# Kernel tuning notes

Measured on AMD Instinct MI355X. Metric: run time of the kernel, lower is better.

## Reference

```python
import jax, jax.numpy as jnp
import numpy as np

L, B, S, D = 8, 1, 4096, 2048
H, KVH, HD = 16, 2, 128
Q = 32
THETA = 1e6
MROPE = (16, 24, 24)  # mrope_section, sums to HD//2
EPS = 1e-6


def setup_inputs() -> dict:
    key = jax.random.key(0)
    ks = jax.random.split(key, 8)
    hidden_states = jax.random.normal(ks[0], (L, B, S, D), dtype=jnp.float32)
    ln_w = jax.random.uniform(ks[1], (L, D), dtype=jnp.float32, minval=0.5, maxval=1.5)
    q_w = jax.random.normal(ks[2], (L, D, H * HD), dtype=jnp.float32) * 0.02
    q_b = jax.random.normal(ks[3], (L, H * HD), dtype=jnp.float32) * 0.02
    k_w = jax.random.normal(ks[4], (L, D, KVH * HD), dtype=jnp.float32) * 0.02
    k_b = jax.random.normal(ks[5], (L, KVH * HD), dtype=jnp.float32) * 0.02
    position_ids = jax.random.randint(ks[6], (3, B, S), 0, S, dtype=jnp.int32)
    q_idx = jnp.sort(jax.random.randint(ks[7], (Q,), 0, S, dtype=jnp.int32))
    return {"hidden_states": hidden_states, "ln_w": ln_w, "q_w": q_w, "q_b": q_b,
            "k_w": k_w, "k_b": k_b, "position_ids": position_ids, "q_idx": q_idx}


def _rot_half(x):
    h = x.shape[-1] // 2
    return jnp.concatenate([-x[..., h:], x[..., :h]], axis=-1)


def _mrope_combine(t):
    # t: (3, B, S, HD). Split last dim per 2*mrope_section, chunk i taken from axis i%3.
    parts, off = [], 0
    for i, sec in enumerate(MROPE):
        w = 2 * sec
        parts.append(t[i % 3, :, :, off:off + w])
        off += w
    return jnp.concatenate(parts, axis=-1)[:, None, :, :]  # (B, 1, S, HD)


def reference(hidden_states, ln_w, q_w, q_b, k_w, k_b, position_ids, q_idx):
    # Rotary embeddings from 3D mRoPE position ids
    inv_freq = 1.0 / (THETA ** (jnp.arange(0, HD, 2, dtype=jnp.float32) / HD))  # (HD/2,)
    freqs = position_ids.astype(jnp.float32)[..., None] * inv_freq  # (3, B, S, HD/2)
    emb = jnp.concatenate([freqs, freqs], axis=-1)  # (3, B, S, HD)
    cos = _mrope_combine(jnp.cos(emb))  # (B, 1, S, HD)
    sin = _mrope_combine(jnp.sin(emb))
    cos_q = cos[:, :, q_idx, :]  # (B, 1, Q, HD)
    sin_q = sin[:, :, q_idx, :]
    # Eager causal mask sliced at query rows: (Q, S)
    mask_add = jnp.where(jnp.arange(S)[None, :] > q_idx[:, None], -1e9, 0.0).astype(jnp.float32)

    scale = 1.0 / np.sqrt(HD).astype(np.float32)

    def per_layer(hs, lw, qw, qb, kw, kb):
        # RMSNorm (input_layernorm)
        var = jnp.mean(jnp.square(hs), axis=-1, keepdims=True)
        x = hs * jax.lax.rsqrt(var + EPS) * lw  # (B, S, D)
        xq = x[:, q_idx, :]  # (B, Q, D)
        k = (jnp.einsum('bsd,de->bse', x, kw) + kb).reshape(B, S, KVH, HD).transpose(0, 2, 1, 3)
        q = (jnp.einsum('bqd,de->bqe', xq, qw) + qb).reshape(B, Q, H, HD).transpose(0, 2, 1, 3)
        k = jnp.repeat(k, H // KVH, axis=1)  # repeat_kv -> (B, H, S, HD)
        k = k * cos + _rot_half(k) * sin
        q = q * cos_q + _rot_half(q) * sin_q
        scores = jnp.einsum('bhqd,bhkd->bhqk', q, k) * scale  # (B, H, Q, S)
        scores = scores + mask_add[None, None]
        return jax.nn.softmax(scores.astype(jnp.float32), axis=-1)

    return jax.vmap(per_layer)(hidden_states, ln_w, q_w, q_b, k_w, k_b)  # (L, B, H, Q, S)
```

## Files before the change

kernel.cpp:

```cpp
#include <hip/hip_runtime.h>
#include <hip/hip_bf16.h>
#include <math.h>

#define LYR 8
#define SEQ 4096
#define DIM 2048
#define NH 16
#define HD 128
#define NQ 32
#define NKV 256
#define NQE 2048

typedef __attribute__((ext_vector_type(8))) short short8;
typedef __attribute__((ext_vector_type(4))) float f32x4;

#define WS_IRQ   0
#define WS_ABLOB 256
#define WS_COS   524544
#define WS_SIN   1048832
#define WS_QBUF  1573120
#define WS_PART  2097408
#define WS_W2    4194560
#define WS_KBLOB 8388864
#define WS_QBLOB 16777472

__device__ __forceinline__ short f2bf(float x) {
  __hip_bfloat16 h = __float2bfloat16(x);
  return *(short*)&h;
}
__device__ __forceinline__ float bf2f(short s) {
  unsigned u = ((unsigned)(unsigned short)s) << 16;
  return __uint_as_float(u);
}

__device__ __forceinline__ void split1(float x, short& h, short& l) {
  unsigned b = __float_as_uint(x);
  h = (short)(b >> 16);
  float lo = x - __uint_as_float(b & 0xffff0000u);
  l = (short)((__float_as_uint(lo) + 0x8000u) >> 16);
}

#define GLOAD16(srcp, dstp) \
  __builtin_amdgcn_global_load_lds( \
      (const __attribute__((address_space(1))) unsigned int*)(srcp), \
      (__attribute__((address_space(3))) unsigned int*)(dstp), 16, 0, 0)

#define RBAR() asm volatile("s_waitcnt lgkmcnt(0)\n\ts_barrier" ::: "memory")

__global__ __launch_bounds__(256) void prep_kernel(
    const float* __restrict__ ln_w, const float* __restrict__ k_w,
    short* __restrict__ W2) {
  int kb = blockIdx.x, l = blockIdx.y, t = threadIdx.x;
  const float* kwl = k_w + (size_t)l * DIM * NKV;
  const float* lnl = ln_w + l * DIM;
  short* blob = W2 + (size_t)(l * 64 + kb) * 16384;
  #pragma unroll
  for (int i = 0; i < 4; ++i) {
    int p = t + i * 256;
    int fi = p >> 6, lane = p & 63;
    int n = fi * 16 + (lane & 15);
    int k0 = kb * 32 + (lane >> 4) * 8;
    short hi8[8], lo8[8];
    #pragma unroll
    for (int e = 0; e < 8; ++e) {
      float v = lnl[k0 + e] * kwl[(size_t)(k0 + e) * NKV + n];
      short h = f2bf(v);
      hi8[e] = h;
      lo8[e] = f2bf(v - bf2f(h));
    }
    *(short8*)(blob + p * 8) = *(short8*)hi8;
    *(short8*)(blob + 8192 + p * 8) = *(short8*)lo8;
  }
}

__global__ __launch_bounds__(256) void rmsq_kernel(const float* __restrict__ hs,
                                                   const int* __restrict__ q_idx,
                                                   float* __restrict__ irq) {
  int qi = blockIdx.x, l = blockIdx.y, t = threadIdx.x;
  int s = q_idx[qi];
  const float* row = hs + ((size_t)l * SEQ + s) * DIM;
  float4 v0 = *(const float4*)(row + t * 4);
  float4 v1 = *(const float4*)(row + t * 4 + 1024);
  float acc = v0.x*v0.x + v0.y*v0.y + v0.z*v0.z + v0.w*v0.w
            + v1.x*v1.x + v1.y*v1.y + v1.z*v1.z + v1.w*v1.w;
  #pragma unroll
  for (int off = 32; off >= 1; off >>= 1) acc += __shfl_down(acc, off);
  __shared__ float red[4];
  if ((t & 63) == 0) red[t >> 6] = acc;
  __syncthreads();
  if (t == 0) {
    float tot = red[0] + red[1] + red[2] + red[3];
    irq[l * NQ + qi] = rsqrtf(tot / (float)DIM + 1e-6f);
  }
}

__global__ void cossin_kernel(const int* __restrict__ pos_ids,
                              float* __restrict__ cost, float* __restrict__ sint) {
  int idx = blockIdx.x * 256 + threadIdx.x;
  int s = idx >> 7, d = idx & 127;
  int t = (d < 32) ? 0 : (d < 80 ? 1 : 2);
  int j = d & 63;
  double invf = pow(1000000.0, -(double)j / 64.0);
  double ph = (double)pos_ids[t * SEQ + s] * invf;
  cost[idx] = (float)cos(ph);
  sint[idx] = (float)sin(ph);
}

__global__ __launch_bounds__(256) void xqt_kernel(
    const float* __restrict__ hs, const float* __restrict__ ln_w,
    const int* __restrict__ q_idx, const float* __restrict__ irq,
    short* __restrict__ Ablob) {
  __shared__ int qix[32];
  __shared__ float qir[32];
  int l = blockIdx.x, t = threadIdx.x;
  if (t < 32) { qix[t] = q_idx[t]; qir[t] = irq[l * NQ + t]; }
  __syncthreads();
  int lane = t & 63, g4 = t >> 6;
  short* base = Ablob + (size_t)l * 131072;
  int row = lane & 15, kgl = lane >> 4;
  for (int i = 0; i < 64; ++i) {
    int group = g4 * 64 + i;
    int kb = group >> 2, half = (group >> 1) & 1, mf = group & 1;
    int r = row + mf * 16;
    int k0 = kb * 32 + kgl * 8;
    const float* src = hs + ((size_t)l * SEQ + qix[r]) * DIM + k0;
    const float* lnp = ln_w + l * DIM + k0;
    float ir = qir[r];
    float4 v0 = *(const float4*)src;
    float4 v1 = *(const float4*)(src + 4);
    float4 w0 = *(const float4*)lnp;
    float4 w1 = *(const float4*)(lnp + 4);
    float av[8] = {v0.x*w0.x, v0.y*w0.y, v0.z*w0.z, v0.w*w0.w,
                   v1.x*w1.x, v1.y*w1.y, v1.z*w1.z, v1.w*w1.w};
    short o8[8];
    #pragma unroll
    for (int e = 0; e < 8; ++e) {
      float v = av[e] * ir;
      short hh, ll;
      split1(v, hh, ll);
      o8[e] = half ? ll : hh;
    }
    *(short8*)(base + group * 512 + lane * 8) = *(short8*)o8;
  }
}

__global__ __launch_bounds__(256) void kgemm_kernel(
    const float* __restrict__ hs, const short* __restrict__ W2,
    const float* __restrict__ k_b, const float* __restrict__ cost,
    const float* __restrict__ sint, short* __restrict__ Kblob) {
  __shared__ __align__(1024) char SM[66816];

  int t = threadIdx.x;
  int fid = blockIdx.x;
  int l = fid & 7, sb = fid >> 3;
  int s0 = sb * 64;
  int lane = t & 63, w = t >> 6;
  int fr = lane & 15, kg = lane >> 4;
  int arow = t >> 2, akg = t & 3;

  const float* hrow = hs + ((size_t)l * SEQ + s0 + arow) * DIM + akg * 8;
  const char* wbase = (const char*)(W2 + (size_t)l * 64 * 16384);
  const char* wfrag = wbase + w * 1024 + lane * 16;

  int awoff = (arow >> 4) * 1024 + (((akg * 16 + (arow & 15)) * 16) ^ (akg << 5));
  int aroff = (lane * 16) ^ ((lane >> 4) << 5);

  f32x4 acc[4][4];
  #pragma unroll
  for (int mf = 0; mf < 4; ++mf)
    #pragma unroll
    for (int nf = 0; nf < 4; ++nf) acc[mf][nf] = (f32x4){0.f, 0.f, 0.f, 0.f};
  float sq = 0.f;
  short8 B0h[4], B0l[4], B1h[4], B1l[4];

  #pragma unroll
  for (int s = 0; s < 4; ++s) {
    float4 a0 = *(const float4*)(hrow + s * 32);
    float4 a1 = *(const float4*)(hrow + s * 32 + 4);
    float av[8] = {a0.x, a0.y, a0.z, a0.w, a1.x, a1.y, a1.z, a1.w};
    short hi8[8], lo8[8];
    #pragma unroll
    for (int e = 0; e < 8; ++e) {
      sq = fmaf(av[e], av[e], sq);
      split1(av[e], hi8[e], lo8[e]);
    }
    *(short8*)(SM + s * 8192 + awoff) = *(short8*)hi8;
    *(short8*)(SM + s * 8192 + 4096 + awoff) = *(short8*)lo8;
  }
  #pragma unroll
  for (int nf = 0; nf < 4; ++nf) {
    B0h[nf] = *(const short8*)(wfrag + nf * 4096);
    B0l[nf] = *(const short8*)(wfrag + nf * 4096 + 16384);
  }
  RBAR();

  for (int ch = 0; ch < 16; ++ch) {
    int buf = ch & 1;
    const char* abuf = SM + buf * 32768;
    char* anext = SM + (buf ^ 1) * 32768;

    float4 cA[8];
    if (ch < 15) {
      #pragma unroll
      for (int s = 0; s < 4; ++s) {
        cA[s * 2]     = *(const float4*)(hrow + (ch + 1) * 128 + s * 32);
        cA[s * 2 + 1] = *(const float4*)(hrow + (ch + 1) * 128 + s * 32 + 4);
      }
    }

    #pragma unroll
    for (int s = 0; s < 4; ++s) {
      if (s < 3 || ch < 15) {
        const char* bsrc = wfrag + (size_t)(ch * 4 + s + 1) * 32768;
        if ((s & 1) == 0) {
          #pragma unroll
          for (int nf = 0; nf < 4; ++nf) {
            B1h[nf] = *(const short8*)(bsrc + nf * 4096);
            B1l[nf] = *(const short8*)(bsrc + nf * 4096 + 16384);
          }
        } else {
          #pragma unroll
          for (int nf = 0; nf < 4; ++nf) {
            B0h[nf] = *(const short8*)(bsrc + nf * 4096);
            B0l[nf] = *(const short8*)(bsrc + nf * 4096 + 16384);
          }
        }
      }
      short8 ah[4], al[4];
      #pragma unroll
      for (int mf = 0; mf < 4; ++mf) {
        ah[mf] = *(const short8*)(abuf + s * 8192 + mf * 1024 + aroff);
        al[mf] = *(const short8*)(abuf + s * 8192 + 4096 + mf * 1024 + aroff);
      }
      __builtin_amdgcn_s_setprio(1);
      if ((s & 1) == 0) {
        #pragma unroll
        for (int nf = 0; nf < 4; ++nf)
          #pragma unroll
          for (int mf = 0; mf < 4; ++mf)
            acc[mf][nf] = __builtin_amdgcn_mfma_f32_16x16x32_bf16(ah[mf], B0h[nf], acc[mf][nf], 0, 0, 0);
        #pragma unroll
        for (int nf = 0; nf < 4; ++nf)
          #pragma unroll
          for (int mf = 0; mf < 4; ++mf)
            acc[mf][nf] = __builtin_amdgcn_mfma_f32_16x16x32_bf16(ah[mf], B0l[nf], acc[mf][nf], 0, 0, 0);
        #pragma unroll
        for (int nf = 0; nf < 4; ++nf)
          #pragma unroll
          for (int mf = 0; mf < 4; ++mf)
            acc[mf][nf] = __builtin_amdgcn_mfma_f32_16x16x32_bf16(al[mf], B0h[nf], acc[mf][nf], 0, 0, 0);
      } else {
        #pragma unroll
        for (int nf = 0; nf < 4; ++nf)
          #pragma unroll
          for (int mf = 0; mf < 4; ++mf)
            acc[mf][nf] = __builtin_amdgcn_mfma_f32_16x16x32_bf16(ah[mf], B1h[nf], acc[mf][nf], 0, 0, 0);
        #pragma unroll
        for (int nf = 0; nf < 4; ++nf)
          #pragma unroll
          for (int mf = 0; mf < 4; ++mf)
            acc[mf][nf] = __builtin_amdgcn_mfma_f32_16x16x32_bf16(ah[mf], B1l[nf], acc[mf][nf], 0, 0, 0);
        #pragma unroll
        for (int nf = 0; nf < 4; ++nf)
          #pragma unroll
          for (int mf = 0; mf < 4; ++mf)
            acc[mf][nf] = __builtin_amdgcn_mfma_f32_16x16x32_bf16(al[mf], B1h[nf], acc[mf][nf], 0, 0, 0);
      }
      __builtin_amdgcn_s_setprio(0);
    }

    if (ch < 15) {
      #pragma unroll
      for (int s = 0; s < 4; ++s) {
        float4 a0 = cA[s * 2];
        float4 a1 = cA[s * 2 + 1];
        float av[8] = {a0.x, a0.y, a0.z, a0.w, a1.x, a1.y, a1.z, a1.w};
        short hi8[8], lo8[8];
        #pragma unroll
        for (int e = 0; e < 8; ++e) {
          sq = fmaf(av[e], av[e], sq);
          split1(av[e], hi8[e], lo8[e]);
        }
        *(short8*)(anext + s * 8192 + awoff) = *(short8*)hi8;
        *(short8*)(anext + s * 8192 + 4096 + awoff) = *(short8*)lo8;
      }
    }
    RBAR();
  }

  sq += __shfl_xor(sq, 1);
  sq += __shfl_xor(sq, 2);
  float* irs = (float*)(SM + 66560);
  if ((t & 3) == 0) irs[arow] = rsqrtf(sq / (float)DIM + 1e-6f);
  __syncthreads();

  float* Kraw = (float*)SM;
  int j = w * 16 + fr;
  float bias0 = k_b[l * NKV + j];
  float bias1 = k_b[l * NKV + j + 64];
  float bias2 = k_b[l * NKV + j + 128];
  float bias3 = k_b[l * NKV + j + 192];
  #pragma unroll
  for (int mf = 0; mf < 4; ++mf) {
    #pragma unroll
    for (int r = 0; r < 4; ++r) {
      int row = mf * 16 + kg * 4 + r;
      int s = s0 + row;
      float ir = irs[row];
      float v0 = acc[mf][0][r] * ir + bias0;
      float v1 = acc[mf][1][r] * ir + bias1;
      float v2 = acc[mf][2][r] * ir + bias2;
      float v3 = acc[mf][3][r] * ir + bias3;
      float cj = cost[s * HD + j], sj = sint[s * HD + j];
      float cj2 = cost[s * HD + j + 64], sj2 = sint[s * HD + j + 64];
      float* kr = Kraw + row * 260;
      kr[j]       = v0 * cj - v1 * sj;
      kr[j + 64]  = v1 * cj2 + v0 * sj2;
      kr[j + 128] = v2 * cj - v3 * sj;
      kr[j + 192] = v3 * cj2 + v2 * sj2;
    }
  }
  __syncthreads();

  int kc = sb >> 1, fb = (sb & 1) * 4;
  #pragma unroll
  for (int i = 0; i < 8; ++i) {
    int c = t + i * 256;
    int lc = c & 63, fl = (c >> 6) & 3, ts = (c >> 8) & 3, kv = c >> 10;
    int key = fl * 16 + (lc & 15);
    int d0 = kv * 128 + ts * 32 + (lc >> 4) * 8;
    float4 x0 = *(const float4*)(Kraw + key * 260 + d0);
    float4 x1 = *(const float4*)(Kraw + key * 260 + d0 + 4);
    float av[8] = {x0.x, x0.y, x0.z, x0.w, x1.x, x1.y, x1.z, x1.w};
    short hi8[8], lo8[8];
    #pragma unroll
    for (int e = 0; e < 8; ++e) split1(av[e], hi8[e], lo8[e]);
    short* bb = Kblob + (size_t)((l * 2 + kv) * 32 + kc) * 32768
              + (size_t)((ts * 2 + 0) * 8 + fb + fl) * 512 + lc * 8;
    *(short8*)bb = *(short8*)hi8;
    *(short8*)(bb + 4096) = *(short8*)lo8;
  }
}

__global__ __launch_bounds__(512) void qgemm_kernel(
    const float* __restrict__ q_w, const short* __restrict__ Ablob,
    float* __restrict__ part) {
  __shared__ __align__(1024) char SM[131072];
  int t = threadIdx.x;
  int nc = blockIdx.x, ks = blockIdx.y, l = blockIdx.z;
  int lane = t & 63, w = t >> 6;
  int fr = lane & 15, kg = lane >> 4;
  const char* abase = (const char*)(Ablob + (size_t)l * 131072 + (size_t)ks * 32768);
  const float* qwl = q_w + (size_t)l * DIM * NQE;

  #pragma unroll
  for (int c = 0; c < 8; ++c) {
    int chunk = w * 8 + c;
    GLOAD16(abase + chunk * 1024 + lane * 16, SM + chunk * 1024);
  }
  #pragma unroll
  for (int c = 0; c < 4; ++c) {
    int r = w * 4 + c;
    GLOAD16((const char*)(qwl + (size_t)(ks * 512 + r) * NQE + nc * 256) + lane * 16,
            SM + 65536 + r * 1024 + lane * 16);
  }
  f32x4 acc[2][2];
  #pragma unroll
  for (int mf = 0; mf < 2; ++mf)
    #pragma unroll
    for (int nf = 0; nf < 2; ++nf) acc[mf][nf] = (f32x4){0.f, 0.f, 0.f, 0.f};
  __syncthreads();

  for (int ts = 0; ts < 16; ++ts) {
    int buf = ts & 1;
    if (ts < 15) {
      #pragma unroll
      for (int c = 0; c < 4; ++c) {
        int r = w * 4 + c;
        GLOAD16((const char*)(qwl + (size_t)(ks * 512 + (ts + 1) * 32 + r) * NQE + nc * 256) + lane * 16,
                SM + 65536 + (buf ^ 1) * 32768 + r * 1024 + lane * 16);
      }
    }
    short8 ah[2], al[2];
    #pragma unroll
    for (int mf = 0; mf < 2; ++mf) {
      ah[mf] = *(const short8*)(SM + ts * 4096 + mf * 1024 + lane * 16);
      al[mf] = *(const short8*)(SM + ts * 4096 + 2048 + mf * 1024 + lane * 16);
    }
    const float* bt = (const float*)(SM + 65536 + buf * 32768);
    short8 bh[2], bl[2];
    #pragma unroll
    for (int nf = 0; nf < 2; ++nf) {
      int c = w * 32 + nf * 16 + fr;
      short bh8[8], bl8[8];
      #pragma unroll
      for (int e = 0; e < 8; ++e) {
        float v = bt[(kg * 8 + e) * 256 + c];
        split1(v, bh8[e], bl8[e]);
      }
      bh[nf] = *(short8*)bh8;
      bl[nf] = *(short8*)bl8;
    }
    #pragma unroll
    for (int nf = 0; nf < 2; ++nf)
      #pragma unroll
      for (int mf = 0; mf < 2; ++mf)
        acc[mf][nf] = __builtin_amdgcn_mfma_f32_16x16x32_bf16(ah[mf], bh[nf], acc[mf][nf], 0, 0, 0);
    #pragma unroll
    for (int nf = 0; nf < 2; ++nf)
      #pragma unroll
      for (int mf = 0; mf < 2; ++mf)
        acc[mf][nf] = __builtin_amdgcn_mfma_f32_16x16x32_bf16(ah[mf], bl[nf], acc[mf][nf], 0, 0, 0);
    #pragma unroll
    for (int nf = 0; nf < 2; ++nf)
      #pragma unroll
      for (int mf = 0; mf < 2; ++mf)
        acc[mf][nf] = __builtin_amdgcn_mfma_f32_16x16x32_bf16(al[mf], bh[nf], acc[mf][nf], 0, 0, 0);
    __syncthreads();
  }

  #pragma unroll
  for (int mf = 0; mf < 2; ++mf) {
    #pragma unroll
    for (int r = 0; r < 4; ++r) {
      int row = mf * 16 + kg * 4 + r;
      float* prow = part + ((size_t)((ks * LYR + l) * NQ + row)) * NQE + nc * 256;
      #pragma unroll
      for (int nf = 0; nf < 2; ++nf) {
        int col = w * 32 + nf * 16 + fr;
        prow[col] = acc[mf][nf][r];
      }
    }
  }
}

__global__ __launch_bounds__(256) void qred_kernel(
    const float* __restrict__ part, const float* __restrict__ q_b,
    float* __restrict__ Qbuf) {
  int idx = blockIdx.x * 256 + threadIdx.x;
  int n = idx & 2047, q = (idx >> 11) & 31, l = idx >> 16;
  float v = q_b[l * NQE + n];
  #pragma unroll
  for (int ks = 0; ks < 4; ++ks)
    v += part[((size_t)((ks * LYR + l) * NQ + q)) * NQE + n];
  Qbuf[((size_t)l * NQ + q) * NQE + n] = v;
}

__global__ __launch_bounds__(256) void qpack_kernel(
    const float* __restrict__ Qbuf, const float* __restrict__ cost,
    const float* __restrict__ sint, const int* __restrict__ q_idx,
    short* __restrict__ Qblob) {
  int kv = blockIdx.x, l = blockIdx.y, t = threadIdx.x;
  short* blob = Qblob + (size_t)(l * 2 + kv) * 65536;
  #pragma unroll
  for (int i = 0; i < 16; ++i) {
    int p = t + i * 256;
    int ts = p >> 10, f = (p >> 6) & 15, lane = p & 63;
    int row = f * 16 + (lane & 15);
    int hh = row >> 5, q = row & 31;
    int h = kv * 8 + hh;
    int d0 = ts * 32 + (lane >> 4) * 8;
    int s = q_idx[q];
    const float* qrow = Qbuf + ((size_t)l * NQ + q) * NQE + h * HD;
    const float* ct = cost + s * HD;
    const float* st = sint + s * HD;
    short hi8[8], lo8[8];
    #pragma unroll
    for (int e = 0; e < 8; ++e) {
      int d = d0 + e;
      float x = qrow[d];
      float xp = qrow[d ^ 64];
      float v = (d < 64) ? (x * ct[d] - xp * st[d]) : (x * ct[d] + xp * st[d]);
      split1(v, hi8[e], lo8[e]);
    }
    *(short8*)(blob + ((ts * 2 + 0) * 16 + f) * 512 + lane * 8) = *(short8*)hi8;
    *(short8*)(blob + ((ts * 2 + 1) * 16 + f) * 512 + lane * 8) = *(short8*)lo8;
  }
}

__global__ __launch_bounds__(512) void scores_kernel(
    const short* __restrict__ Qblob, const short* __restrict__ Kblob,
    const int* __restrict__ q_idx, float* __restrict__ out) {
  __shared__ short Qs[2][16384];
  __shared__ short Ks[2][8192];
  __shared__ int qiv[32];
  int t = threadIdx.x;
  int kc = blockIdx.x, kv = blockIdx.y, l = blockIdx.z;
  int lane = t & 63, w = t >> 6;
  int wm = w >> 1, wn = w & 1;
  if (t < 32) qiv[t] = q_idx[t];
  const char* qsrc = (const char*)(Qblob + (size_t)(l * 2 + kv) * 65536);
  const char* ksrc = (const char*)(Kblob + (size_t)((l * 2 + kv) * 32 + kc) * 32768);
  #pragma unroll
  for (int c = 0; c < 4; ++c) {
    int off = (w * 4 + c) * 1024;
    GLOAD16(qsrc + off + lane * 16, (char*)Qs[0] + off);
  }
  #pragma unroll
  for (int c = 0; c < 2; ++c) {
    int off = (w * 2 + c) * 1024;
    GLOAD16(ksrc + off + lane * 16, (char*)Ks[0] + off);
  }
  f32x4 acc[4][4];
  #pragma unroll
  for (int mf = 0; mf < 4; ++mf)
    #pragma unroll
    for (int nf = 0; nf < 4; ++nf) acc[mf][nf] = (f32x4){0.f, 0.f, 0.f, 0.f};
  __syncthreads();
  for (int ts = 0; ts < 4; ++ts) {
    int buf = ts & 1;
    if (ts < 3) {
      const char* qs = qsrc + (ts + 1) * 32768;
      const char* ks = ksrc + (ts + 1) * 16384;
      #pragma unroll
      for (int c = 0; c < 4; ++c) {
        int off = (w * 4 + c) * 1024;
        GLOAD16(qs + off + lane * 16, (char*)Qs[(ts + 1) & 1] + off);
      }
      #pragma unroll
      for (int c = 0; c < 2; ++c) {
        int off = (w * 2 + c) * 1024;
        GLOAD16(ks + off + lane * 16, (char*)Ks[(ts + 1) & 1] + off);
      }
    }
    short8 ah[4], al[4];
    #pragma unroll
    for (int mf = 0; mf < 4; ++mf) {
      int f = wm * 4 + mf;
      ah[mf] = *(const short8*)(Qs[buf] + f * 512 + lane * 8);
      al[mf] = *(const short8*)(Qs[buf] + 8192 + f * 512 + lane * 8);
    }
    short8 bh[4], bl[4];
    #pragma unroll
    for (int nf = 0; nf < 4; ++nf) {
      int f = wn * 4 + nf;
      bh[nf] = *(const short8*)(Ks[buf] + f * 512 + lane * 8);
      bl[nf] = *(const short8*)(Ks[buf] + 4096 + f * 512 + lane * 8);
    }
    #pragma unroll
    for (int nf = 0; nf < 4; ++nf)
      #pragma unroll
      for (int mf = 0; mf < 4; ++mf)
        acc[mf][nf] = __builtin_amdgcn_mfma_f32_16x16x32_bf16(ah[mf], bh[nf], acc[mf][nf], 0, 0, 0);
    #pragma unroll
    for (int nf = 0; nf < 4; ++nf)
      #pragma unroll
      for (int mf = 0; mf < 4; ++mf)
        acc[mf][nf] = __builtin_amdgcn_mfma_f32_16x16x32_bf16(ah[mf], bl[nf], acc[mf][nf], 0, 0, 0);
    #pragma unroll
    for (int nf = 0; nf < 4; ++nf)
      #pragma unroll
      for (int mf = 0; mf < 4; ++mf)
        acc[mf][nf] = __builtin_amdgcn_mfma_f32_16x16x32_bf16(al[mf], bh[nf], acc[mf][nf], 0, 0, 0);
    __syncthreads();
  }
  const float scale = 0.088388347648318447f;
  #pragma unroll
  for (int mf = 0; mf < 4; ++mf) {
    #pragma unroll
    for (int r = 0; r < 4; ++r) {
      int rr = wm * 64 + mf * 16 + (lane >> 4) * 4 + r;
      int hh = rr >> 5, q = rr & 31;
      int qv = qiv[q];
      float* orow = out + (((size_t)(l * NH + kv * 8 + hh)) * NQ + q) * SEQ;
      #pragma unroll
      for (int nf = 0; nf < 4; ++nf) {
        int key = kc * 128 + (wn * 4 + nf) * 16 + (lane & 15);
        orow[key] = (key > qv) ? -1e9f : acc[mf][nf][r] * scale;
      }
    }
  }
}

__global__ __launch_bounds__(256) void softmax_kernel(float* __restrict__ out) {
  size_t row = blockIdx.x;
  float* p = out + row * SEQ;
  int t = threadIdx.x;
  float4 v[4];
  float mx = -1e30f;
  #pragma unroll
  for (int i = 0; i < 4; ++i) {
    v[i] = *(const float4*)(p + t * 4 + i * 1024);
    mx = fmaxf(mx, fmaxf(fmaxf(v[i].x, v[i].y), fmaxf(v[i].z, v[i].w)));
  }
  #pragma unroll
  for (int off = 32; off >= 1; off >>= 1) mx = fmaxf(mx, __shfl_xor(mx, off));
  __shared__ float red[4];
  if ((t & 63) == 0) red[t >> 6] = mx;
  __syncthreads();
  mx = fmaxf(fmaxf(red[0], red[1]), fmaxf(red[2], red[3]));
  __syncthreads();
  float sum = 0.f;
  #pragma unroll
  for (int i = 0; i < 4; ++i) {
    v[i].x = __expf(v[i].x - mx); v[i].y = __expf(v[i].y - mx);
    v[i].z = __expf(v[i].z - mx); v[i].w = __expf(v[i].w - mx);
    sum += v[i].x + v[i].y + v[i].z + v[i].w;
  }
  #pragma unroll
  for (int off = 32; off >= 1; off >>= 1) sum += __shfl_xor(sum, off);
  if ((t & 63) == 0) red[t >> 6] = sum;
  __syncthreads();
  sum = red[0] + red[1] + red[2] + red[3];
  float inv = 1.f / sum;
  #pragma unroll
  for (int i = 0; i < 4; ++i) {
    v[i].x *= inv; v[i].y *= inv; v[i].z *= inv; v[i].w *= inv;
    *(float4*)(p + t * 4 + i * 1024) = v[i];
  }
}

extern "C" void kernel_launch(void* const* d_in, const int* in_sizes, int n_in,
                              void* d_out, int out_size, void* d_ws, size_t ws_size,
                              hipStream_t stream) {
  const float* hs   = (const float*)d_in[0];
  const float* ln_w = (const float*)d_in[1];
  const float* q_w  = (const float*)d_in[2];
  const float* q_b  = (const float*)d_in[3];
  const float* k_w  = (const float*)d_in[4];
  const float* k_b  = (const float*)d_in[5];
  const int* pos    = (const int*)d_in[6];
  const int* qidx   = (const int*)d_in[7];
  float* out = (float*)d_out;
  float* ws = (float*)d_ws;
  float* irq   = ws + WS_IRQ;
  short* Ablob = (short*)(ws + WS_ABLOB);
  float* cost  = ws + WS_COS;
  float* sint  = ws + WS_SIN;
  float* Qbuf  = ws + WS_QBUF;
  float* part  = ws + WS_PART;
  short* W2    = (short*)(ws + WS_W2);
  short* Kblob = (short*)(ws + WS_KBLOB);
  short* Qblob = (short*)(ws + WS_QBLOB);

  prep_kernel<<<dim3(64, LYR), 256, 0, stream>>>(ln_w, k_w, W2);
  rmsq_kernel<<<dim3(NQ, LYR), 256, 0, stream>>>(hs, qidx, irq);
  cossin_kernel<<<(SEQ * HD) / 256, 256, 0, stream>>>(pos, cost, sint);
  xqt_kernel<<<LYR, 256, 0, stream>>>(hs, ln_w, qidx, irq, Ablob);
  kgemm_kernel<<<512, 256, 0, stream>>>(hs, W2, k_b, cost, sint, Kblob);
  qgemm_kernel<<<dim3(8, 4, LYR), 512, 0, stream>>>(q_w, Ablob, part);
  qred_kernel<<<2048, 256, 0, stream>>>(part, q_b, Qbuf);
  qpack_kernel<<<dim3(2, LYR), 256, 0, stream>>>(Qbuf, cost, sint, qidx, Qblob);
  scores_kernel<<<dim3(32, 2, LYR), 512, 0, stream>>>(Qblob, Kblob, qidx, out);
  softmax_kernel<<<LYR * NH * NQ, 256, 0, stream>>>(out);
}
```

Before: 277.9 us.

## Shrink LDS in kgemm with swizzled staging and re-tile qgemm with register prefetch

kgemm's shared memory is reduced to exactly 64KB by replacing the padded 260-stride K staging buffer with an XOR-swizzled 256-stride layout and holding the per-row rsqrt values in registers. Its s_setprio hints are also removed. qgemm is re-tiled into smaller blocks (256 threads, 128 columns, 8 K-splits, 1024 blocks) that read q_w directly into double-buffered registers instead of staging it through 128KB of LDS, which raises occupancy and parallelism. The cost is more partial sums to reduce, a larger partial workspace, and uncoalesced strided global loads of q_w.

```diff
diff --git a/kernel.cpp b/kernel.cpp
--- a/kernel.cpp
+++ b/kernel.cpp
@@ -20,9 +20,9 @@
 #define WS_SIN   1048832
 #define WS_QBUF  1573120
 #define WS_PART  2097408
-#define WS_W2    4194560
-#define WS_KBLOB 8388864
-#define WS_QBLOB 16777472
+#define WS_W2    6291712
+#define WS_KBLOB 10486016
+#define WS_QBLOB 18874624
 
 __device__ __forceinline__ short f2bf(float x) {
   __hip_bfloat16 h = __float2bfloat16(x);
@@ -148,7 +148,7 @@
     const float* __restrict__ hs, const short* __restrict__ W2,
     const float* __restrict__ k_b, const float* __restrict__ cost,
     const float* __restrict__ sint, short* __restrict__ Kblob) {
-  __shared__ __align__(1024) char SM[66816];
+  __shared__ __align__(1024) char SM[65536];
 
   int t = threadIdx.x;
   int fid = blockIdx.x;
@@ -232,7 +232,6 @@
         ah[mf] = *(const short8*)(abuf + s * 8192 + mf * 1024 + aroff);
         al[mf] = *(const short8*)(abuf + s * 8192 + 4096 + mf * 1024 + aroff);
       }
-      __builtin_amdgcn_s_setprio(1);
       if ((s & 1) == 0) {
         #pragma unroll
         for (int nf = 0; nf < 4; ++nf)
@@ -266,7 +265,6 @@
           for (int mf = 0; mf < 4; ++mf)
             acc[mf][nf] = __builtin_amdgcn_mfma_f32_16x16x32_bf16(al[mf], B1h[nf], acc[mf][nf], 0, 0, 0);
       }
-      __builtin_amdgcn_s_setprio(0);
     }
 
     if (ch < 15) {
@@ -290,11 +288,19 @@
 
   sq += __shfl_xor(sq, 1);
   sq += __shfl_xor(sq, 2);
-  float* irs = (float*)(SM + 66560);
-  if ((t & 3) == 0) irs[arow] = rsqrtf(sq / (float)DIM + 1e-6f);
-  __syncthreads();
-
-  float* Kraw = (float*)SM;
+  float* smf = (float*)SM;
+  __syncthreads();
+  if ((t & 3) == 0) smf[arow] = sq;
+  __syncthreads();
+  float irv[16];
+  #pragma unroll
+  for (int mf = 0; mf < 4; ++mf)
+    #pragma unroll
+    for (int r = 0; r < 4; ++r)
+      irv[mf * 4 + r] = rsqrtf(smf[mf * 16 + kg * 4 + r] / (float)DIM + 1e-6f);
+  __syncthreads();
+
+  float* Kraw = smf;
   int j = w * 16 + fr;
   float bias0 = k_b[l * NKV + j];
   float bias1 = k_b[l * NKV + j + 64];
@@ -306,18 +312,19 @@
     for (int r = 0; r < 4; ++r) {
       int row = mf * 16 + kg * 4 + r;
       int s = s0 + row;
-      float ir = irs[row];
+      float ir = irv[mf * 4 + r];
       float v0 = acc[mf][0][r] * ir + bias0;
       float v1 = acc[mf][1][r] * ir + bias1;
       float v2 = acc[mf][2][r] * ir + bias2;
       float v3 = acc[mf][3][r] * ir + bias3;
       float cj = cost[s * HD + j], sj = sint[s * HD + j];
       float cj2 = cost[s * HD + j + 64], sj2 = sint[s * HD + j + 64];
-      float* kr = Kraw + row * 260;
-      kr[j]       = v0 * cj - v1 * sj;
-      kr[j + 64]  = v1 * cj2 + v0 * sj2;
-      kr[j + 128] = v2 * cj - v3 * sj;
-      kr[j + 192] = v3 * cj2 + v2 * sj2;
+      int sw = (row & 7) << 2;
+      float* kr = Kraw + row * 256;
+      kr[j ^ sw]           = v0 * cj - v1 * sj;
+      kr[(j + 64) ^ sw]    = v1 * cj2 + v0 * sj2;
+      kr[(j + 128) ^ sw]   = v2 * cj - v3 * sj;
+      kr[(j + 192) ^ sw]   = v3 * cj2 + v2 * sj2;
     }
   }
   __syncthreads();
@@ -326,105 +333,109 @@
   #pragma unroll
   for (int i = 0; i < 8; ++i) {
     int c = t + i * 256;
-    int lc = c & 63, fl = (c >> 6) & 3, ts = (c >> 8) & 3, kv = c >> 10;
+    int lc = c & 63, fl = (c >> 6) & 3, ts2 = (c >> 8) & 3, kv = c >> 10;
     int key = fl * 16 + (lc & 15);
-    int d0 = kv * 128 + ts * 32 + (lc >> 4) * 8;
-    float4 x0 = *(const float4*)(Kraw + key * 260 + d0);
-    float4 x1 = *(const float4*)(Kraw + key * 260 + d0 + 4);
+    int d0 = kv * 128 + ts2 * 32 + (lc >> 4) * 8;
+    int sw = (key & 7) << 2;
+    float4 x0 = *(const float4*)(Kraw + key * 256 + (d0 ^ sw));
+    float4 x1 = *(const float4*)(Kraw + key * 256 + ((d0 + 4) ^ sw));
     float av[8] = {x0.x, x0.y, x0.z, x0.w, x1.x, x1.y, x1.z, x1.w};
     short hi8[8], lo8[8];
     #pragma unroll
     for (int e = 0; e < 8; ++e) split1(av[e], hi8[e], lo8[e]);
     short* bb = Kblob + (size_t)((l * 2 + kv) * 32 + kc) * 32768
-              + (size_t)((ts * 2 + 0) * 8 + fb + fl) * 512 + lc * 8;
+              + (size_t)((ts2 * 2 + 0) * 8 + fb + fl) * 512 + lc * 8;
     *(short8*)bb = *(short8*)hi8;
     *(short8*)(bb + 4096) = *(short8*)lo8;
   }
 }
 
-__global__ __launch_bounds__(512) void qgemm_kernel(
+__global__ __launch_bounds__(256) void qgemm_kernel(
     const float* __restrict__ q_w, const short* __restrict__ Ablob,
     float* __restrict__ part) {
-  __shared__ __align__(1024) char SM[131072];
+  __shared__ __align__(1024) char SM[32768];
   int t = threadIdx.x;
   int nc = blockIdx.x, ks = blockIdx.y, l = blockIdx.z;
   int lane = t & 63, w = t >> 6;
   int fr = lane & 15, kg = lane >> 4;
-  const char* abase = (const char*)(Ablob + (size_t)l * 131072 + (size_t)ks * 32768);
-  const float* qwl = q_w + (size_t)l * DIM * NQE;
-
-  #pragma unroll
-  for (int c = 0; c < 8; ++c) {
-    int chunk = w * 8 + c;
-    GLOAD16(abase + chunk * 1024 + lane * 16, SM + chunk * 1024);
-  }
-  #pragma unroll
-  for (int c = 0; c < 4; ++c) {
-    int r = w * 4 + c;
-    GLOAD16((const char*)(qwl + (size_t)(ks * 512 + r) * NQE + nc * 256) + lane * 16,
-            SM + 65536 + r * 1024 + lane * 16);
+  const char* abase = (const char*)(Ablob + (size_t)l * 131072 + (size_t)ks * 16384);
+  const float* bp = q_w + (size_t)l * DIM * NQE + nc * 128 + w * 32 + fr;
+
+  #pragma unroll
+  for (int i = 0; i < 8; ++i) {
+    int c = t + i * 256;
+    GLOAD16(abase + c * 16, SM + c * 16);
   }
   f32x4 acc[2][2];
   #pragma unroll
   for (int mf = 0; mf < 2; ++mf)
     #pragma unroll
     for (int nf = 0; nf < 2; ++nf) acc[mf][nf] = (f32x4){0.f, 0.f, 0.f, 0.f};
-  __syncthreads();
-
-  for (int ts = 0; ts < 16; ++ts) {
-    int buf = ts & 1;
-    if (ts < 15) {
-      #pragma unroll
-      for (int c = 0; c < 4; ++c) {
-        int r = w * 4 + c;
-        GLOAD16((const char*)(qwl + (size_t)(ks * 512 + (ts + 1) * 32 + r) * NQE + nc * 256) + lane * 16,
-                SM + 65536 + (buf ^ 1) * 32768 + r * 1024 + lane * 16);
-      }
-    }
-    short8 ah[2], al[2];
-    #pragma unroll
-    for (int mf = 0; mf < 2; ++mf) {
-      ah[mf] = *(const short8*)(SM + ts * 4096 + mf * 1024 + lane * 16);
-      al[mf] = *(const short8*)(SM + ts * 4096 + 2048 + mf * 1024 + lane * 16);
-    }
-    const float* bt = (const float*)(SM + 65536 + buf * 32768);
-    short8 bh[2], bl[2];
-    #pragma unroll
-    for (int nf = 0; nf < 2; ++nf) {
-      int c = w * 32 + nf * 16 + fr;
-      short bh8[8], bl8[8];
-      #pragma unroll
-      for (int e = 0; e < 8; ++e) {
-        float v = bt[(kg * 8 + e) * 256 + c];
-        split1(v, bh8[e], bl8[e]);
-      }
-      bh[nf] = *(short8*)bh8;
-      bl[nf] = *(short8*)bl8;
-    }
-    #pragma unroll
-    for (int nf = 0; nf < 2; ++nf)
-      #pragma unroll
-      for (int mf = 0; mf < 2; ++mf)
-        acc[mf][nf] = __builtin_amdgcn_mfma_f32_16x16x32_bf16(ah[mf], bh[nf], acc[mf][nf], 0, 0, 0);
-    #pragma unroll
-    for (int nf = 0; nf < 2; ++nf)
-      #pragma unroll
-      for (int mf = 0; mf < 2; ++mf)
-        acc[mf][nf] = __builtin_amdgcn_mfma_f32_16x16x32_bf16(ah[mf], bl[nf], acc[mf][nf], 0, 0, 0);
-    #pragma unroll
-    for (int nf = 0; nf < 2; ++nf)
-      #pragma unroll
-      for (int mf = 0; mf < 2; ++mf)
-        acc[mf][nf] = __builtin_amdgcn_mfma_f32_16x16x32_bf16(al[mf], bh[nf], acc[mf][nf], 0, 0, 0);
-    __syncthreads();
-  }
+
+  float B0[16], B1[16];
+  #pragma unroll
+  for (int nf = 0; nf < 2; ++nf)
+    #pragma unroll
+    for (int e = 0; e < 8; ++e)
+      B0[nf * 8 + e] = bp[(size_t)(ks * 256 + kg * 8 + e) * NQE + nf * 16];
+  __syncthreads();
+
+#define QSTEP(TS, CUR, NXT) do { \
+    if ((TS) < 7) { \
+      _Pragma("unroll") \
+      for (int nf = 0; nf < 2; ++nf) \
+        _Pragma("unroll") \
+        for (int e = 0; e < 8; ++e) \
+          NXT[nf * 8 + e] = bp[(size_t)(ks * 256 + ((TS) + 1) * 32 + kg * 8 + e) * NQE + nf * 16]; \
+    } \
+    short8 ah_[2], al_[2]; \
+    _Pragma("unroll") \
+    for (int mf = 0; mf < 2; ++mf) { \
+      ah_[mf] = *(const short8*)(SM + (TS) * 4096 + mf * 1024 + lane * 16); \
+      al_[mf] = *(const short8*)(SM + (TS) * 4096 + 2048 + mf * 1024 + lane * 16); \
+    } \
+    short8 bh_[2], bl_[2]; \
+    _Pragma("unroll") \
+    for (int nf = 0; nf < 2; ++nf) { \
+      short bh8_[8], bl8_[8]; \
+      _Pragma("unroll") \
+      for (int e = 0; e < 8; ++e) split1(CUR[nf * 8 + e], bh8_[e], bl8_[e]); \
+      bh_[nf] = *(short8*)bh8_; \
+      bl_[nf] = *(short8*)bl8_; \
+    } \
+    _Pragma("unroll") \
+    for (int nf = 0; nf < 2; ++nf) \
+      _Pragma("unroll") \
+      for (int mf = 0; mf < 2; ++mf) \
+        acc[mf][nf] = __builtin_amdgcn_mfma_f32_16x16x32_bf16(ah_[mf], bh_[nf], acc[mf][nf], 0, 0, 0); \
+    _Pragma("unroll") \
+    for (int nf = 0; nf < 2; ++nf) \
+      _Pragma("unroll") \
+      for (int mf = 0; mf < 2; ++mf) \
+        acc[mf][nf] = __builtin_amdgcn_mfma_f32_16x16x32_bf16(ah_[mf], bl_[nf], acc[mf][nf], 0, 0, 0); \
+    _Pragma("unroll") \
+    for (int nf = 0; nf < 2; ++nf) \
+      _Pragma("unroll") \
+      for (int mf = 0; mf < 2; ++mf) \
+        acc[mf][nf] = __builtin_amdgcn_mfma_f32_16x16x32_bf16(al_[mf], bh_[nf], acc[mf][nf], 0, 0, 0); \
+  } while (0)
+
+  QSTEP(0, B0, B1);
+  QSTEP(1, B1, B0);
+  QSTEP(2, B0, B1);
+  QSTEP(3, B1, B0);
+  QSTEP(4, B0, B1);
+  QSTEP(5, B1, B0);
+  QSTEP(6, B0, B1);
+  QSTEP(7, B1, B0);
+#undef QSTEP
 
   #pragma unroll
   for (int mf = 0; mf < 2; ++mf) {
     #pragma unroll
     for (int r = 0; r < 4; ++r) {
       int row = mf * 16 + kg * 4 + r;
-      float* prow = part + ((size_t)((ks * LYR + l) * NQ + row)) * NQE + nc * 256;
+      float* prow = part + ((size_t)((ks * LYR + l) * NQ + row)) * NQE + nc * 128;
       #pragma unroll
       for (int nf = 0; nf < 2; ++nf) {
         int col = w * 32 + nf * 16 + fr;
@@ -441,7 +452,7 @@
   int n = idx & 2047, q = (idx >> 11) & 31, l = idx >> 16;
   float v = q_b[l * NQE + n];
   #pragma unroll
-  for (int ks = 0; ks < 4; ++ks)
+  for (int ks = 0; ks < 8; ++ks)
     v += part[((size_t)((ks * LYR + l) * NQ + q)) * NQE + n];
   Qbuf[((size_t)l * NQ + q) * NQE + n] = v;
 }
@@ -638,7 +649,7 @@
   cossin_kernel<<<(SEQ * HD) / 256, 256, 0, stream>>>(pos, cost, sint);
   xqt_kernel<<<LYR, 256, 0, stream>>>(hs, ln_w, qidx, irq, Ablob);
   kgemm_kernel<<<512, 256, 0, stream>>>(hs, W2, k_b, cost, sint, Kblob);
-  qgemm_kernel<<<dim3(8, 4, LYR), 512, 0, stream>>>(q_w, Ablob, part);
+  qgemm_kernel<<<dim3(16, 8, LYR), 256, 0, stream>>>(q_w, Ablob, part);
   qred_kernel<<<2048, 256, 0, stream>>>(part, q_b, Qbuf);
   qpack_kernel<<<dim3(2, LYR), 256, 0, stream>>>(Qbuf, cost, sint, qidx, Qblob);
   scores_kernel<<<dim3(32, 2, LYR), 512, 0, stream>>>(Qblob, Kblob, qidx, out);
```

Result: slower. 295.9 us (+6.5%).
